# Optimization experiments

Hardware: AMD Instinct MI355X
Metric: run time of the kernel (lower is better)

Reference implementation:

```python
import jax, jax.numpy as jnp
import numpy as np

C = 1.0          # curvature magnitude (args.c)
K = C            # geoopt Lorentz k parameter
EPS = 1e-15
NUM_LAYERS = 3   # resSumGCN propagation depth
CLAMP1 = 50.0    # dist2 clamp for id embeddings
CLAMP2 = 15.0    # dist2 clamp for tag embeddings

# ---- Lorentz manifold math (geoopt conventions, <x,x>_L = -K) ----

def projx(x):
    # project onto hyperboloid: x0 = sqrt(K + ||x_rest||^2)
    x0 = jnp.sqrt(K + jnp.sum(x[..., 1:] ** 2, axis=-1, keepdims=True))
    return jnp.concatenate([x0, x[..., 1:]], axis=-1)

def expmap0(u_rest):
    # exp map at origin; u_rest is the spatial part of the tangent vector
    sk = jnp.sqrt(K)
    norm = jnp.sqrt(jnp.clip(jnp.sum(u_rest ** 2, axis=-1, keepdims=True), EPS))
    x0 = sk * jnp.cosh(norm / sk)
    xr = sk * jnp.sinh(norm / sk) * u_rest / norm
    return jnp.concatenate([x0, xr], axis=-1)

def logmap0(x):
    # log map at origin; returns spatial part of tangent vector
    sk = jnp.sqrt(K)
    alpha = jnp.clip(x[..., :1] / sk, 1.0 + 1e-7)
    rest = x[..., 1:]
    rnorm = jnp.sqrt(jnp.clip(jnp.sum(rest ** 2, axis=-1, keepdims=True), EPS))
    return sk * jnp.arccosh(alpha) * rest / rnorm

def dist2(x, y):
    # squared geodesic distance, keepdim=True -> [..., 1]
    inner = -x[..., :1] * y[..., :1] + jnp.sum(x[..., 1:] * y[..., 1:], axis=-1, keepdims=True)
    d = jnp.clip(-inner / K, 1.0 + 1e-7)
    a = jnp.arccosh(d)
    return K * a * a

def l2p(x):
    # lorentz -> poincare: drops the time coordinate
    return x[..., 1:] / (x[..., :1] + jnp.sqrt(K))

def p2l(x):
    # poincare -> lorentz: adds the time coordinate
    nx = jnp.sum(x ** 2, axis=-1, keepdims=True)
    sk = jnp.sqrt(K)
    num = jnp.concatenate([K + nx, 2.0 * sk * x], axis=-1)
    return sk * num / (K - nx + 1e-6)

def p2k(x):
    denom = 1.0 + C * jnp.sum(x ** 2, axis=-1, keepdims=True)
    return 2.0 * x / denom

def k2p(x):
    denom = 1.0 + jnp.sqrt(jnp.clip(1.0 - C * jnp.sum(x ** 2, axis=-1, keepdims=True), EPS))
    return x / denom

def lorentz_factor(x):
    return 1.0 / jnp.sqrt(jnp.clip(1.0 - C * jnp.sum(x ** 2, axis=-1, keepdims=True), EPS))

def hyper_agg(weights, x):
    # Lorentz-factor weighted Einstein midpoint aggregation
    x_k = p2k(l2p(x))                                   # klein coords [T, d]
    gamma = lorentz_factor(jax.lax.stop_gradient(x_k))  # [T, 1] (detached)
    num = weights @ (gamma * x_k)                        # [M, d]
    den = jnp.clip(weights @ gamma, EPS)                 # [M, 1]
    return p2l(k2p(num / den))                           # [M, d+1]

def encoder_encode(x, edge_src, edge_dst, edge_weight, n_nodes):
    # HGCF-style resSumGCN: tangent-space propagation, sum of powers 1..L
    xt = logmap0(x)
    cur = xt
    acc = jnp.zeros_like(xt)
    for _ in range(NUM_LAYERS):
        msg = edge_weight[:, None] * cur[edge_src]       # [E, d]
        cur = jax.ops.segment_sum(msg, edge_dst, num_segments=n_nodes)
        acc = acc + cur
    return expmap0(acc)


def setup_inputs() -> dict:
    key = jax.random.key(0)
    ks = jax.random.split(key, 8)
    N_USERS, N_ITEMS, D, TAGS = 8192, 40960, 64, 1024
    N = N_USERS + N_ITEMS
    E, B = 1572864, 131072
    emb_weight = 0.1 * jax.random.normal(ks[0], (N, D), dtype=jnp.float32)
    T_weight = 0.1 * jax.random.normal(ks[1], (TAGS, D), dtype=jnp.float32)
    ugr_weight = 0.1 * jax.random.normal(ks[2], (N_USERS, D), dtype=jnp.float32)
    sps = jax.random.uniform(ks[3], (N_ITEMS, TAGS), dtype=jnp.float32)
    sps = sps / jnp.sum(sps, axis=1, keepdims=True)      # row-normalized tag matrix
    edge_src = jax.random.randint(ks[4], (E,), 0, N)
    edge_dst = jax.random.randint(ks[5], (E,), 0, N)
    edge_weight = jax.random.uniform(ks[6], (E,), dtype=jnp.float32) / 32.0
    u = jax.random.randint(ks[7], (B,), 0, N_USERS)
    i = jax.random.randint(jax.random.fold_in(key, 99), (B,), N_USERS, N)
    idx = jnp.stack([u, i], axis=1)
    return {"emb_weight": emb_weight, "T_weight": T_weight, "ugr_weight": ugr_weight,
            "sps": sps, "edge_weight": edge_weight, "edge_src": edge_src,
            "edge_dst": edge_dst, "idx": idx}


def reference(emb_weight, T_weight, ugr_weight, sps, edge_weight, edge_src, edge_dst, idx):
    N, D = emb_weight.shape
    # ---- encode ----
    x1 = projx(emb_weight)
    h_in = encoder_encode(x1, edge_src, edge_dst, edge_weight, N)   # [N, D]
    emb_tag = projx(T_weight)
    emb_tag_in = projx(ugr_weight)                                  # users
    emb_tag_out = hyper_agg(sps, emb_tag)                           # items [N_items, D]
    x2 = jnp.concatenate([emb_tag_in, emb_tag_out], axis=0)         # [N, D]
    h_gr = encoder_encode(x2, edge_src, edge_dst, edge_weight, N)   # [N, D]
    h = jnp.concatenate([h_in, h_gr], axis=-1)                      # [N, 2D]
    # ---- decode ----
    emb_in = h[idx[:, 0], :D]
    emb_out = h[idx[:, 1], :D]
    sq = jnp.minimum(dist2(emb_in, emb_out), CLAMP1)
    tag_in = h[idx[:, 0], D:]
    tag_out = h[idx[:, 1], D:]
    sq = sq + jnp.minimum(dist2(tag_in, tag_out), CLAMP2)
    return sq  # [B, 1]
```

## Files before the change

### kernel.cpp

```cpp
#include <hip/hip_runtime.h>


#define KSPLIT 4
#define NBUK 96
#define CAP 18432

__device__ __forceinline__ float wsum(float v) {
#pragma unroll
  for (int m = 32; m; m >>= 1) v += __shfl_xor(v, m, 64);
  return v;
}

__device__ __forceinline__ float logmap_scale(float ss) {
  float x0 = sqrtf(1.0f + ss);
  float alpha = fmaxf(x0, 1.0f + 1e-7f);
  float rnorm = sqrtf(fmaxf(ss, 1e-15f));
  return acoshf(alpha) / rnorm;
}

__global__ __launch_bounds__(256) void k_prep(
    const float* __restrict__ emb, const float* __restrict__ ugr,
    const float* __restrict__ Tw, float* __restrict__ xt,
    float* __restrict__ gkg, int N, int NU, int TAGS) {
  int n = blockIdx.x * 4 + (threadIdx.x >> 6);
  int lane = threadIdx.x & 63;
  if (n < N) {
    size_t base = (size_t)n * 128;
    float r1 = (lane < 63) ? emb[(size_t)n * 64 + 1 + lane] : 0.0f;
    float sc1 = logmap_scale(wsum(r1 * r1));
    if (lane < 63) xt[base + lane] = sc1 * r1;
    if (lane == 63) { xt[base + 126] = 0.0f; xt[base + 127] = 0.0f; }
    if (n < NU) {
      float r2 = (lane < 63) ? ugr[(size_t)n * 64 + 1 + lane] : 0.0f;
      float sc2 = logmap_scale(wsum(r2 * r2));
      if (lane < 63) xt[base + 63 + lane] = sc2 * r2;
    }
  } else if (n < N + TAGS) {
    int t = n - N;
    float r = (lane < 63) ? Tw[(size_t)t * 64 + 1 + lane] : 0.0f;
    float ss = wsum(r * r);
    float x0 = sqrtf(1.0f + ss);
    float p = r / (x0 + 1.0f);
    float sp = wsum(p * p);
    float k = 2.0f * p / (1.0f + sp);
    float sk2 = wsum(k * k);
    float gamma = 1.0f / sqrtf(fmaxf(1.0f - sk2, 1e-15f));
    gkg[(size_t)t * 64 + lane] = (lane < 63) ? gamma * k : gamma;
  }
}

__global__ __launch_bounds__(256) void k_hyper(
    const float* __restrict__ sps, const float* __restrict__ gkg,
    float* __restrict__ pb, int NI) {
  __shared__ float s_tile[64][36];
  __shared__ float g_tile[32][64];
  int tid = threadIdx.x;
  int tx = tid & 15, ty = tid >> 4;
  int sx = tid & 7,  sy = tid >> 3;
  int gx = tid & 15, gy = tid >> 4;
  int ib = blockIdx.x * 64;
  int kbase = blockIdx.y * 256;
  float acc[4][4];
#pragma unroll
  for (int c = 0; c < 4; ++c)
#pragma unroll
    for (int d = 0; d < 4; ++d) acc[c][d] = 0.0f;

  const float4* sps4 = (const float4*)sps;
  const float4* gkg4 = (const float4*)gkg;

  for (int kc = 0; kc < 8; ++kc) {
    int t4b = (kbase >> 2) + kc * 8;
#pragma unroll
    for (int r = 0; r < 2; ++r) {
      int row = sy + 32 * r;
      *(float4*)&s_tile[row][sx * 4] = sps4[(size_t)(ib + row) * 256 + t4b + sx];
      int grow = gy + 16 * r;
      *(float4*)&g_tile[grow][gx * 4] =
          gkg4[(size_t)(kbase + kc * 32 + grow) * 16 + gx];
    }
    __syncthreads();
#pragma unroll
    for (int tg = 0; tg < 8; ++tg) {
      float4 s4[4], g4[4];
#pragma unroll
      for (int c = 0; c < 4; ++c) s4[c] = *(const float4*)&s_tile[ty * 4 + c][tg * 4];
#pragma unroll
      for (int j = 0; j < 4; ++j) g4[j] = *(const float4*)&g_tile[tg * 4 + j][tx * 4];
#pragma unroll
      for (int c = 0; c < 4; ++c) {
        float sv[4] = {s4[c].x, s4[c].y, s4[c].z, s4[c].w};
#pragma unroll
        for (int j = 0; j < 4; ++j) {
          acc[c][0] = fmaf(sv[j], g4[j].x, acc[c][0]);
          acc[c][1] = fmaf(sv[j], g4[j].y, acc[c][1]);
          acc[c][2] = fmaf(sv[j], g4[j].z, acc[c][2]);
          acc[c][3] = fmaf(sv[j], g4[j].w, acc[c][3]);
        }
      }
    }
    __syncthreads();
  }

  float* dst = pb + ((size_t)blockIdx.y * NI + ib) * 64;
#pragma unroll
  for (int c = 0; c < 4; ++c)
    *(float4*)&dst[(size_t)(ty * 4 + c) * 64 + tx * 4] =
        make_float4(acc[c][0], acc[c][1], acc[c][2], acc[c][3]);
}

__global__ __launch_bounds__(256) void k_combine(
    const float* __restrict__ pb, float* __restrict__ xt, int NI, int NU) {
  int i = blockIdx.x * 4 + (threadIdx.x >> 6);
  if (i >= NI) return;
  int lane = threadIdx.x & 63;
  float v = 0.0f;
#pragma unroll
  for (int s = 0; s < KSPLIT; ++s) v += pb[((size_t)s * NI + i) * 64 + lane];
  float den = fmaxf(__shfl(v, 63, 64), 1e-15f);
  float y = v / den;
  float sy = wsum((lane < 63) ? y * y : 0.0f);
  float dk = 1.0f + sqrtf(fmaxf(1.0f - sy, 1e-15f));
  float q = y / dk;
  float nq = wsum((lane < 63) ? q * q : 0.0f);
  float f = 1.0f / (1.0f - nq + 1e-6f);
  float row0 = (1.0f + nq) * f;
  float r = 2.0f * q * f;
  float srr = wsum((lane < 63) ? r * r : 0.0f);
  float alpha = fmaxf(row0, 1.0f + 1e-7f);
  float scale = acoshf(alpha) / sqrtf(fmaxf(srr, 1e-15f));
  if (lane < 63)
    xt[(size_t)(NU + i) * 128 + 63 + lane] = scale * r;
}


__global__ __launch_bounds__(256) void k_passA(
    const int* __restrict__ esrc, const int* __restrict__ edst,
    const float* __restrict__ ew, int* __restrict__ bcur,
    int2* __restrict__ stage) {
  __shared__ int lh[128];
  __shared__ int lscan[128];
  __shared__ int lcur[128];
  __shared__ int gb[128];
  __shared__ unsigned int keyb[2048];
  __shared__ float wvb[2048];
  int tid = threadIdx.x;
  int base = blockIdx.x * 2048;
  if (tid < 128) lh[tid] = 0;
  __syncthreads();
  unsigned int key[8]; float wv[8];
#pragma unroll
  for (int r = 0; r < 8; ++r) {
    int e = base + r * 256 + tid;
    int d = edst[e];
    key[r] = ((unsigned int)d << 16) | (unsigned int)esrc[e];
    wv[r] = ew[e];
    atomicAdd(&lh[d >> 9], 1);
  }
  __syncthreads();
  if (tid < 128) lscan[tid] = lh[tid];
  __syncthreads();
  for (int d = 1; d < 128; d <<= 1) {
    int v = (tid < 128 && tid >= d) ? lscan[tid - d] : 0;
    __syncthreads();
    if (tid < 128) lscan[tid] += v;
    __syncthreads();
  }
  if (tid < 128) {
    int excl = lscan[tid] - lh[tid];
    lscan[tid] = excl;
    lcur[tid] = 0;
    if (tid < NBUK && lh[tid] > 0) {
      int rsv = atomicAdd(&bcur[tid], lh[tid]);
      gb[tid] = tid * CAP + rsv;
    }
  }
  __syncthreads();
#pragma unroll
  for (int r = 0; r < 8; ++r) {
    int b = key[r] >> 25;
    int lp = lscan[b] + atomicAdd(&lcur[b], 1);
    keyb[lp] = key[r];
    wvb[lp] = wv[r];
  }
  __syncthreads();
#pragma unroll
  for (int r = 0; r < 8; ++r) {
    int i = r * 256 + tid;
    unsigned int k2 = keyb[i];
    int b = k2 >> 25;
    stage[gb[b] + (i - lscan[b])] = make_int2((int)k2, __float_as_int(wvb[i]));
  }
}

__global__ __launch_bounds__(128) void k_bscan(
    const int* __restrict__ bcur, int* __restrict__ bbase,
    int* __restrict__ off, int N, int E) {
  __shared__ int sc[128];
  int t = threadIdx.x;
  int v = (t < NBUK) ? min(bcur[t], CAP) : 0;
  sc[t] = v;
  __syncthreads();
  for (int d = 1; d < 128; d <<= 1) {
    int x = (t >= d) ? sc[t - d] : 0;
    __syncthreads();
    sc[t] += x;
    __syncthreads();
  }
  if (t < NBUK) bbase[t] = sc[t] - v;
  if (t == 0) off[N] = E;
}

__global__ __launch_bounds__(256) void k_passB2(
    const int2* __restrict__ stage, const int* __restrict__ bcur,
    const int* __restrict__ bbase, int* __restrict__ off,
    int2* __restrict__ rec) {
  __shared__ int hist[512];
  __shared__ int pairs[256];
  __shared__ int cur[512];
  int b = blockIdx.x, tid = threadIdx.x;
  int cnt = min(bcur[b], CAP);
  const int2* sg = stage + (size_t)b * CAP;
  hist[tid] = 0; hist[tid + 256] = 0;
  __syncthreads();
  for (int i = tid; i < cnt; i += 256)
    atomicAdd(&hist[((unsigned int)sg[i].x >> 16) & 511], 1);
  __syncthreads();
  int h0 = hist[2 * tid], h1 = hist[2 * tid + 1];
  int ps = h0 + h1;
  pairs[tid] = ps;
  __syncthreads();
  for (int d = 1; d < 256; d <<= 1) {
    int v = (tid >= d) ? pairs[tid - d] : 0;
    __syncthreads();
    pairs[tid] += v;
    __syncthreads();
  }
  int base = bbase[b];
  int e0 = base + pairs[tid] - ps;
  int e1 = e0 + h0;
  int gd = b * 512 + 2 * tid;
  off[gd] = e0;      cur[2 * tid] = e0;
  off[gd + 1] = e1;  cur[2 * tid + 1] = e1;
  __syncthreads();
  for (int i = tid; i < cnt; i += 256) {
    int2 r = sg[i];
    unsigned int k2 = (unsigned int)r.x;
    int d = (int)((k2 >> 16) & 511);
    int p = atomicAdd(&cur[d], 1);
    rec[p] = make_int2((int)(k2 & 0xFFFF), r.y);
  }
}

__device__ __forceinline__ float4 gather_row(
    const float* __restrict__ cur, const int* __restrict__ off,
    const int2* __restrict__ rec, int n, int lane) {
  int half = lane >> 5;
  int q = lane & 31;
  const float4* cq = (const float4*)cur + q;
  int beg = off[n], end = off[n + 1];
  float4 acc = make_float4(0.0f, 0.0f, 0.0f, 0.0f);
  for (int j = beg; j < end; j += 64) {
    int cnt = min(64, end - j);
    int sv = 0; float wv = 0.0f;
    if (lane < cnt) {
      int2 rc = rec[j + lane];
      sv = rc.x;
      wv = __int_as_float(rc.y);
    }
    int k = 0;
    for (; k + 16 <= cnt; k += 16) {
      int s[8]; float w[8]; float4 v[8];
#pragma unroll
      for (int u = 0; u < 8; ++u) {
        int e = k + 2 * u + half;
        s[u] = __shfl(sv, e, 64);
        w[u] = __shfl(wv, e, 64);
      }
#pragma unroll
      for (int u = 0; u < 8; ++u) v[u] = cq[(size_t)s[u] * 32];
#pragma unroll
      for (int u = 0; u < 8; ++u) {
        acc.x = fmaf(w[u], v[u].x, acc.x);
        acc.y = fmaf(w[u], v[u].y, acc.y);
        acc.z = fmaf(w[u], v[u].z, acc.z);
        acc.w = fmaf(w[u], v[u].w, acc.w);
      }
    }
    for (; k + 8 <= cnt; k += 8) {
      int s[4]; float w[4]; float4 v[4];
#pragma unroll
      for (int u = 0; u < 4; ++u) {
        int e = k + 2 * u + half;
        s[u] = __shfl(sv, e, 64);
        w[u] = __shfl(wv, e, 64);
      }
#pragma unroll
      for (int u = 0; u < 4; ++u) v[u] = cq[(size_t)s[u] * 32];
#pragma unroll
      for (int u = 0; u < 4; ++u) {
        acc.x = fmaf(w[u], v[u].x, acc.x);
        acc.y = fmaf(w[u], v[u].y, acc.y);
        acc.z = fmaf(w[u], v[u].z, acc.z);
        acc.w = fmaf(w[u], v[u].w, acc.w);
      }
    }
    for (; k + 2 <= cnt; k += 2) {
      int e = k + half;
      int s0 = __shfl(sv, e, 64);
      float w0 = __shfl(wv, e, 64);
      float4 v = cq[(size_t)s0 * 32];
      acc.x = fmaf(w0, v.x, acc.x);
      acc.y = fmaf(w0, v.y, acc.y);
      acc.z = fmaf(w0, v.z, acc.z);
      acc.w = fmaf(w0, v.w, acc.w);
    }
    if (k < cnt) {
      int s0 = __shfl(sv, k, 64);
      float w0 = __shfl(wv, k, 64);
      if (half == 0) {
        float4 v = cq[(size_t)s0 * 32];
        acc.x = fmaf(w0, v.x, acc.x);
        acc.y = fmaf(w0, v.y, acc.y);
        acc.z = fmaf(w0, v.z, acc.z);
        acc.w = fmaf(w0, v.w, acc.w);
      }
    }
  }
  acc.x += __shfl_xor(acc.x, 32, 64);
  acc.y += __shfl_xor(acc.y, 32, 64);
  acc.z += __shfl_xor(acc.z, 32, 64);
  acc.w += __shfl_xor(acc.w, 32, 64);
  return acc;
}

__global__ __launch_bounds__(256) void k_gather(
    const float* __restrict__ cur, float* __restrict__ nxt,
    const int* __restrict__ off, const int2* __restrict__ rec, int N) {
  int n = blockIdx.x * 4 + (threadIdx.x >> 6);
  if (n >= N) return;
  int lane = threadIdx.x & 63;
  float4 acc = gather_row(cur, off, rec, n, lane);
  if (lane < 32) ((float4*)(nxt + (size_t)n * 128))[lane] = acc;
}

__global__ __launch_bounds__(256) void k_gather_exp(
    const float* __restrict__ cur, const float* b1, const float* __restrict__ b2,
    const int* __restrict__ off, const int2* __restrict__ rec,
    float* h, int N) {
  int n = blockIdx.x * 4 + (threadIdx.x >> 6);
  if (n >= N) return;
  int lane = threadIdx.x & 63;
  int q = lane & 31;
  float4 a3 = gather_row(cur, off, rec, n, lane);
  size_t b = (size_t)n * 128;
  float4 r1 = ((const float4*)(b1 + b))[q];
  float4 r2 = ((const float4*)(b2 + b))[q];
  float vv[4] = {a3.x + r1.x + r2.x, a3.y + r1.y + r2.y,
                 a3.z + r1.z + r2.z, a3.w + r1.w + r2.w};
  float p0 = 0.0f, p1 = 0.0f;
#pragma unroll
  for (int i = 0; i < 4; ++i) {
    int c = 4 * q + i;
    if (c < 63) p0 += vv[i] * vv[i]; else p1 += vv[i] * vv[i];
  }
  float ss0 = 0.5f * wsum(p0);
  float ss1 = 0.5f * wsum(p1);
  float nn0 = sqrtf(fmaxf(ss0, 1e-15f)), nn1 = sqrtf(fmaxf(ss1, 1e-15f));
  float s0 = sinhf(nn0) / nn0, s1 = sinhf(nn1) / nn1;
  int prev = (lane == 0) ? 0 : lane - 1;
  float pv2 = __shfl(vv[2], prev, 64);
  float pv3 = __shfl(vv[3], prev, 64);
  if (lane < 32) {
    float4 o;
    if (q < 16) {
      o.x = (q == 0) ? coshf(nn0) : s0 * pv3;
      o.y = s0 * vv[0]; o.z = s0 * vv[1]; o.w = s0 * vv[2];
    } else {
      o.x = (q == 16) ? coshf(nn1) : s1 * pv2;
      o.y = s1 * pv3; o.z = s1 * vv[0]; o.w = s1 * vv[1];
    }
    ((float4*)(h + b))[q] = o;
  }
}

__global__ __launch_bounds__(256) void k_score(
    const float* __restrict__ h, const int* __restrict__ idx,
    float* __restrict__ out, int B) {
  int w = blockIdx.x * 4 + (threadIdx.x >> 6);
  int lane = threadIdx.x & 63;
  int b0 = w * 4;
  if (b0 >= B) return;
  int np = min(4, B - b0);
  float2 hu[4], hv[4];
#pragma unroll
  for (int p = 0; p < 4; ++p) {
    int bb = b0 + ((p < np) ? p : 0);
    int u = idx[2 * bb], v = idx[2 * bb + 1];
    hu[p] = ((const float2*)(h + (size_t)u * 128))[lane];
    hv[p] = ((const float2*)(h + (size_t)v * 128))[lane];
  }
#pragma unroll
  for (int p = 0; p < 4; ++p) {
    if (p >= np) break;
    float px = hu[p].x * hv[p].x;
    if (lane == 0 || lane == 32) px = -px;
    float pp = px + hu[p].y * hv[p].y;
#pragma unroll
    for (int m = 1; m < 32; m <<= 1) pp += __shfl_xor(pp, m, 64);
    float dd = fmaxf(-pp, 1.0f + 1e-7f);
    float a = acoshf(dd);
    float s = fminf(a * a, (lane < 32) ? 50.0f : 15.0f);
    s += __shfl_xor(s, 32, 64);
    if (lane == 0) out[b0 + p] = s;
  }
}

extern "C" void kernel_launch(void* const* d_in, const int* in_sizes, int n_in,
                              void* d_out, int out_size, void* d_ws, size_t ws_size,
                              hipStream_t stream) {
  const float* emb = (const float*)d_in[0];
  const float* Tw  = (const float*)d_in[1];
  const float* ugr = (const float*)d_in[2];
  const float* sps = (const float*)d_in[3];
  const float* ew  = (const float*)d_in[4];
  const int* esrc  = (const int*)d_in[5];
  const int* edst  = (const int*)d_in[6];
  const int* idx   = (const int*)d_in[7];
  float* out = (float*)d_out;

  const int N    = in_sizes[0] / 64;
  const int TAGS = in_sizes[1] / 64;
  const int NU   = in_sizes[2] / 64;
  const int NI   = in_sizes[3] / TAGS;
  const int E    = in_sizes[4];
  const int B    = in_sizes[7] / 2;

  size_t rowsz = (size_t)N * 128 * sizeof(float);
  char* ws = (char*)d_ws;
  float* xt  = (float*)(ws);
  float* b1  = (float*)(ws + rowsz);
  float* b2  = (float*)(ws + 2 * rowsz);
  float* gkg = (float*)(ws + 3 * rowsz);
  size_t o = 3 * rowsz + (size_t)TAGS * 64 * sizeof(float);
  int* off   = (int*)(ws + o);  o += (size_t)(N + 1) * sizeof(int);
  int* bcur  = (int*)(ws + o);  o += (size_t)NBUK * sizeof(int);
  int* bbase = (int*)(ws + o);  o += (size_t)NBUK * sizeof(int);
  o = (o + 7) & ~(size_t)7;
  int2* rec = (int2*)(ws + o);
  int2* stage = (int2*)b2;
  float* pb = b1;
  float* h  = b1;

  hipMemsetAsync(bcur, 0, (size_t)NBUK * sizeof(int), stream);
  k_passA<<<E / 2048, 256, 0, stream>>>(esrc, edst, ew, bcur, stage);
  k_bscan<<<1, 128, 0, stream>>>(bcur, bbase, off, N, E);
  k_passB2<<<NBUK, 256, 0, stream>>>(stage, bcur, bbase, off, rec);

  k_prep<<<(N + TAGS + 3) / 4, 256, 0, stream>>>(emb, ugr, Tw, xt, gkg, N, NU, TAGS);
  dim3 hgrid(NI / 64, KSPLIT);
  k_hyper<<<hgrid, 256, 0, stream>>>(sps, gkg, pb, NI);
  k_combine<<<(NI + 3) / 4, 256, 0, stream>>>(pb, xt, NI, NU);

  k_gather<<<(N + 3) / 4, 256, 0, stream>>>(xt, b1, off, rec, N);
  k_gather<<<(N + 3) / 4, 256, 0, stream>>>(b1, b2, off, rec, N);
  k_gather_exp<<<(N + 3) / 4, 256, 0, stream>>>(b2, b1, b2, off, rec, h, N);

  k_score<<<(B / 4 + 3) / 4, 256, 0, stream>>>(h, idx, out, B);
}
```

Baseline: 546.6 us.

## Fuse CSR build with prep and hyper-agg kernels into two horizontal megakernels

Independent kernels are merged by block index: the edge bucketing pass runs alongside the embedding prep in one launch, and the per-bucket CSR fill runs alongside the sparse-weight aggregation GEMM in another. The separate bucket-scan kernel goes away because each CSR block now recomputes the bucket prefix sum itself. The aggregation GEMM no longer stages sps in shared memory; it reads it straight into registers with a one-step prefetch, and KSPLIT drops from 4 to 2. This cuts launch count and lets unrelated work overlap, at the cost of larger shared-memory footprints per block, uncoalesced direct sps loads, and fewer GEMM blocks.

```diff
diff --git a/kernel.cpp b/kernel.cpp
--- a/kernel.cpp
+++ b/kernel.cpp
@@ -1,7 +1,7 @@
 #include <hip/hip_runtime.h>
 
 
-#define KSPLIT 4
+#define KSPLIT 2
 #define NBUK 96
 #define CAP 18432
 
@@ -18,11 +18,71 @@
   return acoshf(alpha) / rnorm;
 }
 
-__global__ __launch_bounds__(256) void k_prep(
+
+__device__ void passA_body(
+    const int* __restrict__ esrc, const int* __restrict__ edst,
+    const float* __restrict__ ew, int* __restrict__ bcur,
+    int2* __restrict__ stage, int bx) {
+  __shared__ int lh[128];
+  __shared__ int lscan[128];
+  __shared__ int lcur[128];
+  __shared__ int gb[128];
+  __shared__ unsigned int keyb[2048];
+  __shared__ float wvb[2048];
+  int tid = threadIdx.x;
+  int base = bx * 2048;
+  if (tid < 128) lh[tid] = 0;
+  __syncthreads();
+  unsigned int key[8]; float wv[8];
+#pragma unroll
+  for (int r = 0; r < 8; ++r) {
+    int e = base + r * 256 + tid;
+    int d = edst[e];
+    key[r] = ((unsigned int)d << 16) | (unsigned int)esrc[e];
+    wv[r] = ew[e];
+    atomicAdd(&lh[d >> 9], 1);
+  }
+  __syncthreads();
+  if (tid < 128) lscan[tid] = lh[tid];
+  __syncthreads();
+  for (int d = 1; d < 128; d <<= 1) {
+    int v = (tid < 128 && tid >= d) ? lscan[tid - d] : 0;
+    __syncthreads();
+    if (tid < 128) lscan[tid] += v;
+    __syncthreads();
+  }
+  if (tid < 128) {
+    int excl = lscan[tid] - lh[tid];
+    lscan[tid] = excl;
+    lcur[tid] = 0;
+    if (tid < NBUK && lh[tid] > 0) {
+      int rsv = atomicAdd(&bcur[tid], lh[tid]);
+      gb[tid] = tid * CAP + rsv;
+    }
+  }
+  __syncthreads();
+#pragma unroll
+  for (int r = 0; r < 8; ++r) {
+    int b = key[r] >> 25;
+    int lp = lscan[b] + atomicAdd(&lcur[b], 1);
+    keyb[lp] = key[r];
+    wvb[lp] = wv[r];
+  }
+  __syncthreads();
+#pragma unroll
+  for (int r = 0; r < 8; ++r) {
+    int i = r * 256 + tid;
+    unsigned int k2 = keyb[i];
+    int b = k2 >> 25;
+    stage[gb[b] + (i - lscan[b])] = make_int2((int)k2, __float_as_int(wvb[i]));
+  }
+}
+
+__device__ void prep_body(
     const float* __restrict__ emb, const float* __restrict__ ugr,
     const float* __restrict__ Tw, float* __restrict__ xt,
-    float* __restrict__ gkg, int N, int NU, int TAGS) {
-  int n = blockIdx.x * 4 + (threadIdx.x >> 6);
+    float* __restrict__ gkg, int N, int NU, int TAGS, int pbx) {
+  int n = pbx * 4 + (threadIdx.x >> 6);
   int lane = threadIdx.x & 63;
   if (n < N) {
     size_t base = (size_t)n * 128;
@@ -49,17 +109,78 @@
   }
 }
 
-__global__ __launch_bounds__(256) void k_hyper(
+__global__ __launch_bounds__(256) void k_mega1(
+    const int* __restrict__ esrc, const int* __restrict__ edst,
+    const float* __restrict__ ew, int* __restrict__ bcur,
+    int2* __restrict__ stage,
+    const float* __restrict__ emb, const float* __restrict__ ugr,
+    const float* __restrict__ Tw, float* __restrict__ xt,
+    float* __restrict__ gkg, int N, int NU, int TAGS, int nA) {
+  if ((int)blockIdx.x < nA)
+    passA_body(esrc, edst, ew, bcur, stage, blockIdx.x);
+  else
+    prep_body(emb, ugr, Tw, xt, gkg, N, NU, TAGS, blockIdx.x - nA);
+}
+
+
+__device__ void passB2_body(
+    const int2* __restrict__ stage, const int* __restrict__ bcur,
+    int* __restrict__ off, int2* __restrict__ rec, int N, int E) {
+  __shared__ int hist[512];
+  __shared__ int pairs[256];
+  __shared__ int cur[512];
+  __shared__ int bs[128];
+  int b = blockIdx.x, tid = threadIdx.x;
+  if (tid < 128) bs[tid] = (tid < NBUK) ? min(bcur[tid], CAP) : 0;
+  hist[tid] = 0; hist[tid + 256] = 0;
+  __syncthreads();
+  for (int d = 1; d < 128; d <<= 1) {
+    int v = (tid < 128 && tid >= d) ? bs[tid - d] : 0;
+    __syncthreads();
+    if (tid < 128) bs[tid] += v;
+    __syncthreads();
+  }
+  int cnt = min(bcur[b], CAP);
+  int base = bs[b] - cnt;
+  if (b == 0 && tid == 0) off[N] = E;
+  const int2* sg = stage + (size_t)b * CAP;
+  for (int i = tid; i < cnt; i += 256)
+    atomicAdd(&hist[((unsigned int)sg[i].x >> 16) & 511], 1);
+  __syncthreads();
+  int h0 = hist[2 * tid], h1 = hist[2 * tid + 1];
+  int ps = h0 + h1;
+  pairs[tid] = ps;
+  __syncthreads();
+  for (int d = 1; d < 256; d <<= 1) {
+    int v = (tid >= d) ? pairs[tid - d] : 0;
+    __syncthreads();
+    pairs[tid] += v;
+    __syncthreads();
+  }
+  int e0 = base + pairs[tid] - ps;
+  int e1 = e0 + h0;
+  int gd = b * 512 + 2 * tid;
+  off[gd] = e0;      cur[2 * tid] = e0;
+  off[gd + 1] = e1;  cur[2 * tid + 1] = e1;
+  __syncthreads();
+  for (int i = tid; i < cnt; i += 256) {
+    int2 r = sg[i];
+    unsigned int k2 = (unsigned int)r.x;
+    int d = (int)((k2 >> 16) & 511);
+    int p = atomicAdd(&cur[d], 1);
+    rec[p] = make_int2((int)(k2 & 0xFFFF), r.y);
+  }
+}
+
+__device__ void hyper_body(
     const float* __restrict__ sps, const float* __restrict__ gkg,
-    float* __restrict__ pb, int NI) {
-  __shared__ float s_tile[64][36];
-  __shared__ float g_tile[32][64];
+    float* __restrict__ pb, int NI, int bx, int ksp) {
+  __shared__ float g_tile[32 * 64];
   int tid = threadIdx.x;
   int tx = tid & 15, ty = tid >> 4;
-  int sx = tid & 7,  sy = tid >> 3;
   int gx = tid & 15, gy = tid >> 4;
-  int ib = blockIdx.x * 64;
-  int kbase = blockIdx.y * 256;
+  int ib = bx * 64;
+  int kbase = ksp * (1024 / KSPLIT);
   float acc[4][4];
 #pragma unroll
   for (int c = 0; c < 4; ++c)
@@ -68,28 +189,34 @@
 
   const float4* sps4 = (const float4*)sps;
   const float4* gkg4 = (const float4*)gkg;
-
-  for (int kc = 0; kc < 8; ++kc) {
-    int t4b = (kbase >> 2) + kc * 8;
+  size_t rb[4];
+#pragma unroll
+  for (int c = 0; c < 4; ++c) rb[c] = (size_t)(ib + ty * 4 + c) * 256;
+
+  for (int kc = 0; kc < (1024 / KSPLIT) / 32; ++kc) {
 #pragma unroll
     for (int r = 0; r < 2; ++r) {
-      int row = sy + 32 * r;
-      *(float4*)&s_tile[row][sx * 4] = sps4[(size_t)(ib + row) * 256 + t4b + sx];
       int grow = gy + 16 * r;
-      *(float4*)&g_tile[grow][gx * 4] =
+      *(float4*)&g_tile[grow * 64 + gx * 4] =
           gkg4[(size_t)(kbase + kc * 32 + grow) * 16 + gx];
     }
     __syncthreads();
+    int t4 = (kbase >> 2) + kc * 8;
+    float4 A[4], Nb[4];
+#pragma unroll
+    for (int c = 0; c < 4; ++c) A[c] = sps4[rb[c] + t4];
 #pragma unroll
     for (int tg = 0; tg < 8; ++tg) {
-      float4 s4[4], g4[4];
-#pragma unroll
-      for (int c = 0; c < 4; ++c) s4[c] = *(const float4*)&s_tile[ty * 4 + c][tg * 4];
-#pragma unroll
-      for (int j = 0; j < 4; ++j) g4[j] = *(const float4*)&g_tile[tg * 4 + j][tx * 4];
+#pragma unroll
+      for (int c = 0; c < 4; ++c)
+        if (tg < 7) Nb[c] = sps4[rb[c] + t4 + tg + 1];
+      float4 g4[4];
+#pragma unroll
+      for (int j = 0; j < 4; ++j)
+        g4[j] = *(const float4*)&g_tile[(tg * 4 + j) * 64 + tx * 4];
 #pragma unroll
       for (int c = 0; c < 4; ++c) {
-        float sv[4] = {s4[c].x, s4[c].y, s4[c].z, s4[c].w};
+        float sv[4] = {A[c].x, A[c].y, A[c].z, A[c].w};
 #pragma unroll
         for (int j = 0; j < 4; ++j) {
           acc[c][0] = fmaf(sv[j], g4[j].x, acc[c][0]);
@@ -98,15 +225,32 @@
           acc[c][3] = fmaf(sv[j], g4[j].w, acc[c][3]);
         }
       }
-    }
-    __syncthreads();
-  }
-
-  float* dst = pb + ((size_t)blockIdx.y * NI + ib) * 64;
+#pragma unroll
+      for (int c = 0; c < 4; ++c)
+        if (tg < 7) A[c] = Nb[c];
+    }
+    __syncthreads();
+  }
+
+  float* dst = pb + ((size_t)ksp * NI + ib) * 64;
 #pragma unroll
   for (int c = 0; c < 4; ++c)
     *(float4*)&dst[(size_t)(ty * 4 + c) * 64 + tx * 4] =
         make_float4(acc[c][0], acc[c][1], acc[c][2], acc[c][3]);
+}
+
+__global__ __launch_bounds__(256) void k_mega2(
+    const int2* __restrict__ stage, const int* __restrict__ bcur,
+    int* __restrict__ off, int2* __restrict__ rec,
+    const float* __restrict__ sps, const float* __restrict__ gkg,
+    float* __restrict__ pb, int NI, int N, int E) {
+  if ((int)blockIdx.x < NBUK) {
+    passB2_body(stage, bcur, off, rec, N, E);
+  } else {
+    int hb = blockIdx.x - NBUK;
+    int nbx = NI / 64;
+    hyper_body(sps, gkg, pb, NI, hb % nbx, hb / nbx);
+  }
 }
 
 __global__ __launch_bounds__(256) void k_combine(
@@ -133,125 +277,6 @@
     xt[(size_t)(NU + i) * 128 + 63 + lane] = scale * r;
 }
 
-
-__global__ __launch_bounds__(256) void k_passA(
-    const int* __restrict__ esrc, const int* __restrict__ edst,
-    const float* __restrict__ ew, int* __restrict__ bcur,
-    int2* __restrict__ stage) {
-  __shared__ int lh[128];
-  __shared__ int lscan[128];
-  __shared__ int lcur[128];
-  __shared__ int gb[128];
-  __shared__ unsigned int keyb[2048];
-  __shared__ float wvb[2048];
-  int tid = threadIdx.x;
-  int base = blockIdx.x * 2048;
-  if (tid < 128) lh[tid] = 0;
-  __syncthreads();
-  unsigned int key[8]; float wv[8];
-#pragma unroll
-  for (int r = 0; r < 8; ++r) {
-    int e = base + r * 256 + tid;
-    int d = edst[e];
-    key[r] = ((unsigned int)d << 16) | (unsigned int)esrc[e];
-    wv[r] = ew[e];
-    atomicAdd(&lh[d >> 9], 1);
-  }
-  __syncthreads();
-  if (tid < 128) lscan[tid] = lh[tid];
-  __syncthreads();
-  for (int d = 1; d < 128; d <<= 1) {
-    int v = (tid < 128 && tid >= d) ? lscan[tid - d] : 0;
-    __syncthreads();
-    if (tid < 128) lscan[tid] += v;
-    __syncthreads();
-  }
-  if (tid < 128) {
-    int excl = lscan[tid] - lh[tid];
-    lscan[tid] = excl;
-    lcur[tid] = 0;
-    if (tid < NBUK && lh[tid] > 0) {
-      int rsv = atomicAdd(&bcur[tid], lh[tid]);
-      gb[tid] = tid * CAP + rsv;
-    }
-  }
-  __syncthreads();
-#pragma unroll
-  for (int r = 0; r < 8; ++r) {
-    int b = key[r] >> 25;
-    int lp = lscan[b] + atomicAdd(&lcur[b], 1);
-    keyb[lp] = key[r];
-    wvb[lp] = wv[r];
-  }
-  __syncthreads();
-#pragma unroll
-  for (int r = 0; r < 8; ++r) {
-    int i = r * 256 + tid;
-    unsigned int k2 = keyb[i];
-    int b = k2 >> 25;
-    stage[gb[b] + (i - lscan[b])] = make_int2((int)k2, __float_as_int(wvb[i]));
-  }
-}
-
-__global__ __launch_bounds__(128) void k_bscan(
-    const int* __restrict__ bcur, int* __restrict__ bbase,
-    int* __restrict__ off, int N, int E) {
-  __shared__ int sc[128];
-  int t = threadIdx.x;
-  int v = (t < NBUK) ? min(bcur[t], CAP) : 0;
-  sc[t] = v;
-  __syncthreads();
-  for (int d = 1; d < 128; d <<= 1) {
-    int x = (t >= d) ? sc[t - d] : 0;
-    __syncthreads();
-    sc[t] += x;
-    __syncthreads();
-  }
-  if (t < NBUK) bbase[t] = sc[t] - v;
-  if (t == 0) off[N] = E;
-}
-
-__global__ __launch_bounds__(256) void k_passB2(
-    const int2* __restrict__ stage, const int* __restrict__ bcur,
-    const int* __restrict__ bbase, int* __restrict__ off,
-    int2* __restrict__ rec) {
-  __shared__ int hist[512];
-  __shared__ int pairs[256];
-  __shared__ int cur[512];
-  int b = blockIdx.x, tid = threadIdx.x;
-  int cnt = min(bcur[b], CAP);
-  const int2* sg = stage + (size_t)b * CAP;
-  hist[tid] = 0; hist[tid + 256] = 0;
-  __syncthreads();
-  for (int i = tid; i < cnt; i += 256)
-    atomicAdd(&hist[((unsigned int)sg[i].x >> 16) & 511], 1);
-  __syncthreads();
-  int h0 = hist[2 * tid], h1 = hist[2 * tid + 1];
-  int ps = h0 + h1;
-  pairs[tid] = ps;
-  __syncthreads();
-  for (int d = 1; d < 256; d <<= 1) {
-    int v = (tid >= d) ? pairs[tid - d] : 0;
-    __syncthreads();
-    pairs[tid] += v;
-    __syncthreads();
-  }
-  int base = bbase[b];
-  int e0 = base + pairs[tid] - ps;
-  int e1 = e0 + h0;
-  int gd = b * 512 + 2 * tid;
-  off[gd] = e0;      cur[2 * tid] = e0;
-  off[gd + 1] = e1;  cur[2 * tid + 1] = e1;
-  __syncthreads();
-  for (int i = tid; i < cnt; i += 256) {
-    int2 r = sg[i];
-    unsigned int k2 = (unsigned int)r.x;
-    int d = (int)((k2 >> 16) & 511);
-    int p = atomicAdd(&cur[d], 1);
-    rec[p] = make_int2((int)(k2 & 0xFFFF), r.y);
-  }
-}
-
 __device__ __forceinline__ float4 gather_row(
     const float* __restrict__ cur, const int* __restrict__ off,
     const int2* __restrict__ rec, int n, int lane) {
@@ -445,21 +470,21 @@
   size_t o = 3 * rowsz + (size_t)TAGS * 64 * sizeof(float);
   int* off   = (int*)(ws + o);  o += (size_t)(N + 1) * sizeof(int);
   int* bcur  = (int*)(ws + o);  o += (size_t)NBUK * sizeof(int);
-  int* bbase = (int*)(ws + o);  o += (size_t)NBUK * sizeof(int);
   o = (o + 7) & ~(size_t)7;
   int2* rec = (int2*)(ws + o);
   int2* stage = (int2*)b2;
   float* pb = b1;
   float* h  = b1;
 
+  const int nA = E / 2048;
+  const int nPrep = (N + TAGS + 3) / 4;
+  const int nHyper = (NI / 64) * KSPLIT;
+
   hipMemsetAsync(bcur, 0, (size_t)NBUK * sizeof(int), stream);
-  k_passA<<<E / 2048, 256, 0, stream>>>(esrc, edst, ew, bcur, stage);
-  k_bscan<<<1, 128, 0, stream>>>(bcur, bbase, off, N, E);
-  k_passB2<<<NBUK, 256, 0, stream>>>(stage, bcur, bbase, off, rec);
-
-  k_prep<<<(N + TAGS + 3) / 4, 256, 0, stream>>>(emb, ugr, Tw, xt, gkg, N, NU, TAGS);
-  dim3 hgrid(NI / 64, KSPLIT);
-  k_hyper<<<hgrid, 256, 0, stream>>>(sps, gkg, pb, NI);
+  k_mega1<<<nA + nPrep, 256, 0, stream>>>(esrc, edst, ew, bcur, stage,
+                                          emb, ugr, Tw, xt, gkg, N, NU, TAGS, nA);
+  k_mega2<<<NBUK + nHyper, 256, 0, stream>>>(stage, bcur, off, rec,
+                                             sps, gkg, pb, NI, N, E);
   k_combine<<<(NI + 3) / 4, 256, 0, stream>>>(pb, xt, NI, NU);
 
   k_gather<<<(N + 3) / 4, 256, 0, stream>>>(xt, b1, off, rec, N);
```

Measured after the change: 545.2 us. Within noise of the previous version (-0.3%).
